# Performance work log

Hardware: AMD Instinct MI355X
Metric: run time of the kernel (lower is better)

## Reference

```python
import jax, jax.numpy as jnp
import numpy as np

IN_C = 256
INTER_C = 64  # in_c // k, k=4
B, H, W = 8, 32, 32
N_TERMS = 5   # numSeriesTerms; numTraceSamples = 1


def setup_inputs():
    key = jax.random.key(0)
    ks = jax.random.split(key, 10)
    s = 0.05
    return {
        "x": jax.random.normal(ks[0], (B, IN_C, H, W), jnp.float32),
        "Wq": jax.random.normal(ks[1], (INTER_C, IN_C), jnp.float32) * s,
        "bq": jax.random.normal(ks[2], (INTER_C,), jnp.float32) * s,
        "Wk": jax.random.normal(ks[3], (INTER_C, IN_C), jnp.float32) * s,
        "bk": jax.random.normal(ks[4], (INTER_C,), jnp.float32) * s,
        "Wc": jax.random.normal(ks[5], (2 * INTER_C,), jnp.float32) * s,
        "Wv": jax.random.normal(ks[6], (IN_C, IN_C), jnp.float32) * s,
        "bv": jax.random.normal(ks[7], (IN_C,), jnp.float32) * s,
        "gamma": jnp.full((1,), 0.5, jnp.float32),
        "u": jax.random.normal(ks[8], (B, IN_C, H, W), jnp.float32),
    }


def _attention(x, Wq, bq, Wk, bk, Wc, Wv, bv, gamma):
    # Attention_concat.forward. concat_conv is a bias-free linear map over the
    # channel concat, so energy[i,j] = <Wc[:ic], q_i> + <Wc[ic:], k_j> exactly.
    b, c, h, w = x.shape
    n = h * w
    xf = x.reshape(b, c, n)                                   # [B,C,N]
    q = jnp.einsum('oc,bcn->bon', Wq, xf) + bq[None, :, None]  # [B,ic,N]
    k = jnp.einsum('oc,bcn->bon', Wk, xf) + bk[None, :, None]  # [B,ic,N]
    ic = Wq.shape[0]
    eq = jnp.einsum('c,bcn->bn', Wc[:ic], q)                  # [B,N]
    ek = jnp.einsum('c,bcn->bn', Wc[ic:], k)                  # [B,N]
    attn = (eq[:, :, None] + ek[:, None, :]) / n              # energy/(H*W), [B,N,N]
    v = jnp.einsum('oc,bcn->bon', Wv, xf) + bv[None, :, None]  # [B,C,N]
    out = jnp.einsum('bcn,bnm->bcm', v, attn).reshape(b, c, h, w)
    return gamma * out + x


def _forward(x, Wq, bq, Wk, bk, Wc, Wv, bv, gamma, u):
    att = lambda z, g: _attention(z, Wq, bq, Wk, bk, Wc, Wv, bv, g)
    # turbulance_hook: runs under torch.no_grad and rescales gamma in-place
    res = att(x, gamma)
    turbu = att(x * 1.0000001, gamma)
    lip = jnp.linalg.norm(turbu - res) / jnp.linalg.norm(x * 1.0000001 - x)
    factor = jax.lax.stop_gradient(jnp.where(lip > 0.9, 0.9 / lip, 1.0))
    gamma_eff = gamma * factor
    Fx, vjp_fn = jax.vjp(lambda z: att(z, gamma_eff), x)
    # power_series_matrix_logarithm_trace: Hutchinson estimate of
    # tr(log(I+J)) ~= sum_j (-1)^{j+1}/j * u^T J^j u, 1 probe, 5 terms
    b = x.shape[0]
    uf = u.reshape(b, -1)
    vcur = u
    tr = jnp.zeros((b,), x.dtype)
    for j in range(1, N_TERMS + 1):
        vcur = vjp_fn(vcur)[0]                 # u^T J^j via repeated vjp
        dot = jnp.sum(vcur.reshape(b, -1) * uf, axis=1)
        tr = tr + ((-1.0) ** (j + 1) / j) * dot
    return x + Fx, tr


def reference(x, Wq, bq, Wk, bk, Wc, Wv, bv, gamma, u):
    return _forward(x, Wq, bq, Wk, bk, Wc, Wv, bv, gamma, u)
```

## Files before the change

### kernel.cpp

```cpp
#include <hip/hip_runtime.h>
#include <math.h>

#define NB 8
#define NC 256
#define NN 1024
#define NICH 64

#define WS_AQ    0
#define WS_AK    256
#define WS_MOM2  520
#define WS_SX    1024
#define WS_XE    3072
#define WS_XK    5120
#define WS_T1P   7424
#define WS_T2P   7488
#define WS_VSU   7680
#define WS_UE    9728
#define WS_VEU   11776
#define WS_CAQ   13824
#define WS_CAK   15872
#define WS_CUAK  17920
#define WS_STAT  20480
#define STAT_STRIDE 2560
#define ST_EK    1024
#define ST_SV    2048
#define ST_SVE   2304
#define WS_EQP2  57344
#define WS_EKP2  73728
#define WS_MAQP2 90112
#define WS_MAKP2 106496
#define WS_SX2P  123904
#define WS_UUP   124160
#define WS_WVB   124416

__device__ __forceinline__ float dot4(const float4& a, const float4& b) {
    return a.x * b.x + a.y * b.y + a.z * b.z + a.w * b.w;
}
__device__ __forceinline__ float sum4(const float4& a) {
    return a.x + a.y + a.z + a.w;
}
__device__ __forceinline__ unsigned int bf16lo(float v) {
    unsigned int u = __float_as_uint(v);
    return (u + 0x7FFFu + ((u >> 16) & 1u)) >> 16;
}
__device__ __forceinline__ unsigned int bf16hi(float v) {
    unsigned int u = __float_as_uint(v);
    return (u + 0x7FFFu + ((u >> 16) & 1u)) & 0xFFFF0000u;
}
__device__ __forceinline__ float tolo(unsigned int u) {
    return __uint_as_float(u << 16);
}
__device__ __forceinline__ float tohi(unsigned int u) {
    return __uint_as_float(u & 0xFFFF0000u);
}

__global__ void kA(const float* __restrict__ x, const float* __restrict__ u,
                   const float* __restrict__ Wq, const float* __restrict__ Wk,
                   const float* __restrict__ Wc, const float* __restrict__ Wv,
                   float* __restrict__ ws) {
    const int bid = blockIdx.x;
    const int t = threadIdx.x;
    if (bid >= 256) {
        const int j = bid - 256;
        unsigned int* wvb = (unsigned int*)ws + WS_WVB;
#pragma unroll
        for (int r = 0; r < 4; ++r) {
            int e = j * 1024 + r * 256 + t;
            int q = e >> 13, i = (e >> 8) & 31, o = e & 255;
            float w0 = Wv[(size_t)(q * 64 + 2 * i) * NC + o];
            float w1 = Wv[(size_t)(q * 64 + 2 * i + 1) * NC + o];
            wvb[e] = bf16lo(w0) | bf16hi(w1);
        }
        return;
    }
    const int b = bid >> 5, r = bid & 31;
    const int nq = r >> 1, ch = r & 1;
    __shared__ float aql[128], akl[128];
    __shared__ float red[4][4][64];
    {
        const int c_local = t >> 1, half = t & 1;
        const int cg = ch * 128 + c_local;
        float a = 0.f, k = 0.f;
#pragma unroll 8
        for (int i = 0; i < 32; ++i) {
            int o = half * 32 + i;
            a += Wc[o] * Wq[o * NC + cg];
            k += Wc[64 + o] * Wk[o * NC + cg];
        }
        a += __shfl_xor(a, 1, 64);
        k += __shfl_xor(k, 1, 64);
        if (half == 0) {
            aql[c_local] = a; akl[c_local] = k;
            if (nq == 0) { ws[WS_AQ + cg] = a; ws[WS_AK + cg] = k; }
        }
    }
    __syncthreads();
    const int col = t & 63, grp = t >> 6;
    const int n = nq * 64 + col;
    const float* xb = x + ((size_t)b * NC + ch * 128 + grp * 32) * NN + n;
    const float* ub = u + ((size_t)b * NC + ch * 128 + grp * 32) * NN + n;
    float eqp = 0.f, ekp = 0.f, map = 0.f, mkp = 0.f;
#pragma unroll 8
    for (int i = 0; i < 32; ++i) {
        float xv = xb[(size_t)i * NN];
        float uv = ub[(size_t)i * NN];
        float a = aql[grp * 32 + i], kk = akl[grp * 32 + i];
        eqp += a * xv; ekp += kk * xv;
        map += a * uv; mkp += kk * uv;
    }
    red[grp][0][col] = eqp; red[grp][1][col] = ekp;
    red[grp][2][col] = map; red[grp][3][col] = mkp;
    __syncthreads();
    if (t < 64) {
        int idx = (b * 2 + ch) * 1024 + nq * 64 + t;
        ws[WS_EQP2  + idx] = red[0][0][t] + red[1][0][t] + red[2][0][t] + red[3][0][t];
        ws[WS_EKP2  + idx] = red[0][1][t] + red[1][1][t] + red[2][1][t] + red[3][1][t];
        ws[WS_MAQP2 + idx] = red[0][2][t] + red[1][2][t] + red[2][2][t] + red[3][2][t];
        ws[WS_MAKP2 + idx] = red[0][3][t] + red[1][3][t] + red[2][3][t] + red[3][3][t];
    }
}

__global__ void kB(const float* __restrict__ x, const float* __restrict__ u,
                   const float* __restrict__ Wc, const float* __restrict__ bq,
                   const float* __restrict__ bk, float* __restrict__ ws) {
    const int bid = blockIdx.x;
    const int b = bid >> 5, g = bid & 31;
    const int c0 = g * 8;
    const int t = threadIdx.x;
    const int wid = t >> 6, lane = t & 63;
    __shared__ float s_cq, s_ck;
    __shared__ float mred[4][4];
    __shared__ float wv9[8][9][4];
    __shared__ float accw[2][4];
    if (t < 64) {
        float p = Wc[t] * bq[t], rr = Wc[64 + t] * bk[t];
        for (int off = 32; off > 0; off >>= 1) {
            p += __shfl_down(p, off, 64);
            rr += __shfl_down(rr, off, 64);
        }
        if (t == 0) { s_cq = p; s_ck = rr; }
    }
    __syncthreads();
    const float cq = s_cq, ck = s_ck;
    float4 e4, k4, ma4, mk4;
    {
        float4 a0 = ((const float4*)(ws + WS_EQP2 + (size_t)(b * 2) * 1024))[t];
        float4 a1 = ((const float4*)(ws + WS_EQP2 + (size_t)(b * 2 + 1) * 1024))[t];
        e4.x = a0.x + a1.x + cq; e4.y = a0.y + a1.y + cq;
        e4.z = a0.z + a1.z + cq; e4.w = a0.w + a1.w + cq;
        a0 = ((const float4*)(ws + WS_EKP2 + (size_t)(b * 2) * 1024))[t];
        a1 = ((const float4*)(ws + WS_EKP2 + (size_t)(b * 2 + 1) * 1024))[t];
        k4.x = a0.x + a1.x + ck; k4.y = a0.y + a1.y + ck;
        k4.z = a0.z + a1.z + ck; k4.w = a0.w + a1.w + ck;
        a0 = ((const float4*)(ws + WS_MAQP2 + (size_t)(b * 2) * 1024))[t];
        a1 = ((const float4*)(ws + WS_MAQP2 + (size_t)(b * 2 + 1) * 1024))[t];
        ma4.x = a0.x + a1.x; ma4.y = a0.y + a1.y; ma4.z = a0.z + a1.z; ma4.w = a0.w + a1.w;
        a0 = ((const float4*)(ws + WS_MAKP2 + (size_t)(b * 2) * 1024))[t];
        a1 = ((const float4*)(ws + WS_MAKP2 + (size_t)(b * 2 + 1) * 1024))[t];
        mk4.x = a0.x + a1.x; mk4.y = a0.y + a1.y; mk4.z = a0.z + a1.z; mk4.w = a0.w + a1.w;
    }
    {
        float d0 = sum4(e4), d1 = sum4(k4), d2 = dot4(k4, k4), d3 = dot4(e4, k4);
        for (int off = 32; off > 0; off >>= 1) {
            d0 += __shfl_down(d0, off, 64);
            d1 += __shfl_down(d1, off, 64);
            d2 += __shfl_down(d2, off, 64);
            d3 += __shfl_down(d3, off, 64);
        }
        if (lane == 0) { mred[0][wid] = d0; mred[1][wid] = d1; mred[2][wid] = d2; mred[3][wid] = d3; }
    }
    __syncthreads();
    if (t == 0)
        for (int m = 0; m < 4; ++m)
            ws[WS_MOM2 + b * 4 + m] = mred[m][0] + mred[m][1] + mred[m][2] + mred[m][3];
    if (g == 0)
        ((float4*)(ws + WS_STAT + b * STAT_STRIDE + ST_EK))[t] = k4;
    const float4* xb4 = (const float4*)(x + ((size_t)b * NC + c0) * NN);
    const float4* ub4 = (const float4*)(u + ((size_t)b * NC + c0) * NN);
    float x2a = 0.f, uua = 0.f;
#pragma unroll
    for (int c = 0; c < 8; ++c) {
        float4 xv = xb4[c * 256 + t];
        float4 uv = ub4[c * 256 + t];
        float d[9];
        d[0] = dot4(xv, e4);
        d[1] = dot4(xv, k4);
        d[2] = sum4(uv);
        d[3] = dot4(uv, e4);
        d[4] = dot4(uv, k4);
        d[5] = dot4(xv, ma4);
        d[6] = dot4(xv, mk4);
        d[7] = dot4(uv, mk4);
        d[8] = sum4(xv);
        x2a += dot4(xv, xv);
        uua += dot4(uv, uv);
        for (int off = 32; off > 0; off >>= 1)
            for (int m = 0; m < 9; ++m) d[m] += __shfl_down(d[m], off, 64);
        if (lane == 0) for (int m = 0; m < 9; ++m) wv9[c][m][wid] = d[m];
    }
    for (int off = 32; off > 0; off >>= 1) {
        x2a += __shfl_down(x2a, off, 64);
        uua += __shfl_down(uua, off, 64);
    }
    if (lane == 0) { accw[0][wid] = x2a; accw[1][wid] = uua; }
    __syncthreads();
    if (t < 8) {
        int c = t;
        float v[9];
        for (int m = 0; m < 9; ++m)
            v[m] = wv9[c][m][0] + wv9[c][m][1] + wv9[c][m][2] + wv9[c][m][3];
        ws[WS_XE   + b * NC + c0 + c] = v[0];
        ws[WS_XK   + b * NC + c0 + c] = v[1];
        ws[WS_VSU  + b * NC + c0 + c] = v[2];
        ws[WS_UE   + b * NC + c0 + c] = v[3];
        ws[WS_VEU  + b * NC + c0 + c] = v[4];
        ws[WS_CAQ  + b * NC + c0 + c] = v[5];
        ws[WS_CAK  + b * NC + c0 + c] = v[6];
        ws[WS_CUAK + b * NC + c0 + c] = v[7];
        ws[WS_SX   + b * NC + c0 + c] = v[8];
    }
    if (t == 0) {
        ws[WS_SX2P + bid] = accw[0][0] + accw[0][1] + accw[0][2] + accw[0][3];
        ws[WS_UUP + bid]  = accw[1][0] + accw[1][1] + accw[1][2] + accw[1][3];
    }
}

__global__ void ksv(const float* __restrict__ Wv, const float* __restrict__ bv,
                    const float* __restrict__ Wc, const float* __restrict__ bq,
                    const float* __restrict__ bk, float* __restrict__ ws) {
    const int bid = blockIdx.x;
    const int b = bid >> 3, oc = bid & 7;
    const int t = threadIdx.x;
    const int o_sub = t >> 3, ks = t & 7;
    const int o = oc * 32 + o_sub;
    __shared__ float sxl[NC], xel[NC];
    __shared__ float T1s[32], T2s[32];
    __shared__ float s_cq, s_ck;
    if (t < 64) {
        float p = Wc[t] * bq[t], rr = Wc[64 + t] * bk[t];
        for (int off = 32; off > 0; off >>= 1) {
            p += __shfl_down(p, off, 64);
            rr += __shfl_down(rr, off, 64);
        }
        if (t == 0) { s_cq = p; s_ck = rr; }
    }
    sxl[t] = ws[WS_SX + b * NC + t];
    xel[t] = ws[WS_XE + b * NC + t];
    __syncthreads();
    const float Seq  = ws[WS_MOM2 + b * 4 + 0];
    const float Sek  = ws[WS_MOM2 + b * 4 + 1];
    const float Sek2 = ws[WS_MOM2 + b * 4 + 2];
    const float cq = s_cq, ck = s_ck;
    float wsx = 0.f, wxe = 0.f;
    const float4* wrow = (const float4*)(Wv + (size_t)o * NC);
#pragma unroll
    for (int i = 0; i < 8; ++i) {
        float4 w4 = wrow[i * 8 + ks];
        int k = i * 32 + ks * 4;
        wsx += w4.x * sxl[k] + w4.y * sxl[k + 1] + w4.z * sxl[k + 2] + w4.w * sxl[k + 3];
        wxe += w4.x * xel[k] + w4.y * xel[k + 1] + w4.z * xel[k + 2] + w4.w * xel[k + 3];
    }
    for (int off = 4; off > 0; off >>= 1) {
        wsx += __shfl_down(wsx, off, 8);
        wxe += __shfl_down(wxe, off, 8);
    }
    if (ks == 0) {
        float bvc = bv[o];
        float Sv  = wsx + (float)NN * bvc;
        float SvL = wsx;
        float Sve = wxe + bvc * Seq;
        float* st = ws + WS_STAT + b * STAT_STRIDE;
        st[ST_SV + o] = Sv; st[ST_SVE + o] = Sve;
        float A = 2.f * Sve - bvc * Seq - cq * Sv;
        float sx = sxl[o];
        float xk = ws[WS_XK + b * NC + o];
        float xkL = xk - ck * sx;
        float T1c = A * sx + Sv * xkL + SvL * xk;
        float SP  = Sek - (float)NN * ck;
        float SP2 = Sek2 - 2.f * ck * Sek + (float)NN * ck * ck;
        float SPQ = Sek2 - ck * Sek;
        float T2c = (float)NN * A * A + Sv * Sv * SP2 + SvL * SvL * Sek2
                  + 2.f * A * Sv * SP + 2.f * A * SvL * Sek + 2.f * Sv * SvL * SPQ;
        T1s[o_sub] = T1c; T2s[o_sub] = T2c;
    }
    __syncthreads();
    if (t == 0) {
        float t1 = 0.f, t2 = 0.f;
        for (int i = 0; i < 32; ++i) { t1 += T1s[i]; t2 += T2s[i]; }
        ws[WS_T1P + bid] = t1;
        ws[WS_T2P + bid] = t2;
    }
}

struct KFSMem {
    unsigned int Wlds[32768];
    unsigned int VVb[NC] __attribute__((aligned(16)));
    float redPR[2048];
    float dred[9][4];
    float gred0[4];
    float gredT[2];
    float sge;
};

__global__ void __launch_bounds__(1024, 4) kfin(
        const float* __restrict__ x, const float* __restrict__ bv,
        const float* __restrict__ gamma, float* __restrict__ ws,
        float* __restrict__ out) {
    __shared__ __align__(16) unsigned char smem_raw[sizeof(KFSMem)];
    KFSMem& S = *(KFSMem*)smem_raw;
    const int bid = blockIdx.x;
    const int t = threadIdx.x;
    const int lane = t & 63;
    const bool is_iter = (bid < 8);
    uint4 stg0, stg1, stg2, stg3, stg4, stg5, stg6, stg7;
    if (is_iter) {
        const uint4* wvb4 = (const uint4*)((const unsigned int*)ws + WS_WVB);
        stg0 = wvb4[0 * 1024 + t]; stg1 = wvb4[1 * 1024 + t];
        stg2 = wvb4[2 * 1024 + t]; stg3 = wvb4[3 * 1024 + t];
        stg4 = wvb4[4 * 1024 + t]; stg5 = wvb4[5 * 1024 + t];
        stg6 = wvb4[6 * 1024 + t]; stg7 = wvb4[7 * 1024 + t];
    }
    {
        float a = 0.f, b1 = 0.f, c1 = 0.f;
        if (t < 256) a = ws[WS_SX2P + t];
        if (t < 64) { b1 = ws[WS_T1P + t]; c1 = ws[WS_T2P + t]; }
        for (int off = 32; off > 0; off >>= 1) {
            a  += __shfl_down(a,  off, 64);
            b1 += __shfl_down(b1, off, 64);
            c1 += __shfl_down(c1, off, 64);
        }
        if (t < 256 && lane == 0) S.gred0[t >> 6] = a;
        if (t == 0) { S.gredT[0] = b1; S.gredT[1] = c1; }
    }
    __syncthreads();
    if (t == 0) {
        float S1 = S.gred0[0] + S.gred0[1] + S.gred0[2] + S.gred0[3];
        float inv = gamma[0] * (1.f / (float)NN);
        float dd = S1 + 2.f * inv * S.gredT[0] + inv * inv * S.gredT[1];
        float lip = sqrtf(dd / S1);
        S.sge = gamma[0] * ((lip > 0.9f) ? (0.9f / lip) : 1.f);
    }
    __syncthreads();
    const float ge = S.sge;

    if (!is_iter) {
        const float gn = ge * (1.f / (float)NN);
        const int r = t >> 8, tc = t & 255;
        const int bid2 = (bid - 8) * 4 + r;
        const int b = bid2 >> 8, c = bid2 & 255;
        const float* st = ws + WS_STAT + b * STAT_STRIDE;
        float sv = st[ST_SV + c], sve = st[ST_SVE + c];
        float4 ek4 = ((const float4*)(st + ST_EK))[tc];
        size_t i4 = (size_t)bid2 * 256 + tc;
        float4 x4 = ((const float4*)x)[i4];
        float4 o;
        o.x = 2.f * x4.x + gn * (sve + ek4.x * sv);
        o.y = 2.f * x4.y + gn * (sve + ek4.y * sv);
        o.z = 2.f * x4.z + gn * (sve + ek4.z * sv);
        o.w = 2.f * x4.w + gn * (sve + ek4.w * sv);
        ((float4*)out)[i4] = o;
        return;
    }

    const int b = bid;
    const int o = t & 255, q = t >> 8;
    const int wid4 = o >> 6;
    ((uint4*)S.Wlds)[0 * 1024 + t] = stg0; ((uint4*)S.Wlds)[1 * 1024 + t] = stg1;
    ((uint4*)S.Wlds)[2 * 1024 + t] = stg2; ((uint4*)S.Wlds)[3 * 1024 + t] = stg3;
    ((uint4*)S.Wlds)[4 * 1024 + t] = stg4; ((uint4*)S.Wlds)[5 * 1024 + t] = stg5;
    ((uint4*)S.Wlds)[6 * 1024 + t] = stg6; ((uint4*)S.Wlds)[7 * 1024 + t] = stg7;
    const float s = ge * (1.f / (float)NN);
    float Svl_r = 0.f, sxl_r = 0.f, xkl_r = 0.f, caql_r = 0.f, cakl_r = 0.f,
          Uel_r = 0.f, Vsul_r = 0.f, bvl_r = 0.f, aql_r = 0.f, akl_r = 0.f,
          veu_r = 0.f, cuak_r = 0.f, vsreg = 0.f, vereg = 0.f;
    if (t < 256) {
        const float* st = ws + WS_STAT + b * STAT_STRIDE;
        Svl_r  = st[ST_SV + t];
        sxl_r  = ws[WS_SX   + b * NC + t];
        xkl_r  = ws[WS_XK   + b * NC + t];
        caql_r = ws[WS_CAQ  + b * NC + t];
        cakl_r = ws[WS_CAK  + b * NC + t];
        Uel_r  = ws[WS_UE   + b * NC + t];
        Vsul_r = ws[WS_VSU  + b * NC + t];
        veu_r  = ws[WS_VEU  + b * NC + t];
        cuak_r = ws[WS_CUAK + b * NC + t];
        aql_r  = ws[WS_AQ + t];
        akl_r  = ws[WS_AK + t];
        bvl_r  = bv[t];
        vsreg = Vsul_r; vereg = veu_r;
        S.VVb[t] = bf16lo(vsreg) | bf16hi(vereg);
    }
    const float Seq  = ws[WS_MOM2 + b * 4 + 0];
    const float Sek  = ws[WS_MOM2 + b * 4 + 1];
    const float Sekq = ws[WS_MOM2 + b * 4 + 3];
    float uu = 0.f;
    for (int g = 0; g < 32; ++g) uu += ws[WS_UUP + b * 32 + g];
    __syncthreads();
    if (t < 256) {
        float d[8] = {Svl_r * cuak_r, aql_r * Vsul_r, akl_r * Vsul_r, akl_r * Uel_r,
                      Svl_r * Vsul_r, Svl_r * veu_r,  Svl_r * aql_r,  Svl_r * akl_r};
        for (int off = 32; off > 0; off >>= 1)
            for (int m = 0; m < 8; ++m) d[m] += __shfl_down(d[m], off, 64);
        if (lane == 0) for (int m = 0; m < 8; ++m) S.dred[m][wid4] = d[m];
    }
    __syncthreads();
    float g2a = 0.f, aqVsu = 0.f, akVsu = 0.f, akUe = 0.f, SvVsu = 0.f, SvVeu = 0.f,
          Svaq = 0.f, Svak = 0.f;
    if (t < 256) {
        g2a   = S.dred[0][0] + S.dred[0][1] + S.dred[0][2] + S.dred[0][3];
        aqVsu = S.dred[1][0] + S.dred[1][1] + S.dred[1][2] + S.dred[1][3];
        akVsu = S.dred[2][0] + S.dred[2][1] + S.dred[2][2] + S.dred[2][3];
        akUe  = S.dred[3][0] + S.dred[3][1] + S.dred[3][2] + S.dred[3][3];
        SvVsu = S.dred[4][0] + S.dred[4][1] + S.dred[4][2] + S.dred[4][3];
        SvVeu = S.dred[5][0] + S.dred[5][1] + S.dred[5][2] + S.dred[5][3];
        Svaq  = S.dred[6][0] + S.dred[6][1] + S.dred[6][2] + S.dred[6][3];
        Svak  = S.dred[7][0] + S.dred[7][1] + S.dred[7][2] + S.dred[7][3];
    }
    __syncthreads();
    const float lam = 1.f + s * Svak;
    float alpha = 1.f, beta = 0.f, gam = 0.f;
    float SxAcc = 0.f, XkAcc = 0.f, CakAcc = 0.f;
    float dot = uu, tr = 0.f;
    const float coef[5] = {1.f, -0.5f, 1.f / 3.f, -0.25f, 0.2f};
    for (int j = 0; j < 5; ++j) {
        float pa = 0.f, ra = 0.f;
#pragma unroll
        for (int kk = 0; kk < 8; ++kk) {
            const int base = (q * 32 + 4 * kk) * 256 + o;
            unsigned int w0 = S.Wlds[base];
            unsigned int w1 = S.Wlds[base + 256];
            unsigned int w2 = S.Wlds[base + 512];
            unsigned int w3 = S.Wlds[base + 768];
            uint4 va = ((const uint4*)S.VVb)[q * 16 + 2 * kk];
            uint4 vb = ((const uint4*)S.VVb)[q * 16 + 2 * kk + 1];
            pa += tolo(w0) * tolo(va.x) + tohi(w0) * tolo(va.y);
            ra += tolo(w0) * tohi(va.x) + tohi(w0) * tohi(va.y);
            pa += tolo(w1) * tolo(va.z) + tohi(w1) * tolo(va.w);
            ra += tolo(w1) * tohi(va.z) + tohi(w1) * tohi(va.w);
            pa += tolo(w2) * tolo(vb.x) + tohi(w2) * tolo(vb.y);
            ra += tolo(w2) * tohi(vb.x) + tohi(w2) * tohi(vb.y);
            pa += tolo(w3) * tolo(vb.z) + tohi(w3) * tolo(vb.w);
            ra += tolo(w3) * tohi(vb.z) + tohi(w3) * tohi(vb.w);
        }
        S.redPR[2 * t] = pa; S.redPR[2 * t + 1] = ra;
        __syncthreads();
        if (t < 256) {
            float Pv = s * (S.redPR[2 * t] + S.redPR[2 * (t + 256)] + S.redPR[2 * (t + 512)] + S.redPR[2 * (t + 768)]);
            float Rv = s * (S.redPR[2 * t + 1] + S.redPR[2 * (t + 256) + 1] + S.redPR[2 * (t + 512) + 1] + S.redPR[2 * (t + 768) + 1]);
            float d[9];
            d[0] = Svl_r * Pv;
            d[1] = Svl_r * Rv;
            d[2] = bvl_r * vsreg;
            d[3] = sxl_r * Pv;
            d[4] = xkl_r * Pv;
            d[5] = caql_r * Pv;
            d[6] = cakl_r * Pv;
            d[7] = Uel_r * Pv;
            d[8] = Vsul_r * Rv;
            for (int off = 32; off > 0; off >>= 1)
                for (int m = 0; m < 9; ++m) d[m] += __shfl_down(d[m], off, 64);
            if (lane == 0) for (int m = 0; m < 9; ++m) S.dred[m][wid4] = d[m];
            __syncthreads();
            float sm[9];
            for (int m = 0; m < 9; ++m)
                sm[m] = S.dred[m][0] + S.dred[m][1] + S.dred[m][2] + S.dred[m][3];
            const float svP = sm[0], svR = sm[1], bvVs = sm[2], sxP = sm[3], xkP = sm[4],
                        caqP = sm[5], cakP = sm[6], ueP = sm[7], vsuR = sm[8];
            const float sB = s * bvVs;
            float St  = s * (alpha * SvVsu + beta * (float)NN + gam * Seq  + Svaq * SxAcc);
            float tek = s * (alpha * SvVeu + beta * Sek        + gam * Sekq + Svaq * XkAcc);
            float uta = s * (alpha * g2a   + beta * akVsu      + gam * akUe + Svaq * CakAcc);
            dot += ueP + caqP + sB * aqVsu + uta + vsuR;
            tr  += coef[j] * dot;
            float nVs = vsreg + Pv * Seq  + aql_r * (sxP + (float)NN * sB) + akl_r * St  + Rv * (float)NN;
            float nVe = vereg + Pv * Sekq + aql_r * (xkP + sB * Sek)       + akl_r * tek + Rv * Sek;
            vsreg = nVs; vereg = nVe;
            S.VVb[t] = bf16lo(nVs) | bf16hi(nVe);
            SxAcc  = lam * SxAcc  + sxP;
            XkAcc  = lam * XkAcc  + xkP;
            CakAcc = lam * CakAcc + cakP;
            beta = lam * beta + Svaq * sB + svR;
            gam  = lam * gam + svP;
            alpha *= lam;
        } else {
            __syncthreads();
        }
        __syncthreads();
    }
    if (t == 0) out[2097152 + b] = tr;
}

extern "C" void kernel_launch(void* const* d_in, const int* in_sizes, int n_in,
                              void* d_out, int out_size, void* d_ws, size_t ws_size,
                              hipStream_t stream) {
    const float* x     = (const float*)d_in[0];
    const float* Wq    = (const float*)d_in[1];
    const float* bq    = (const float*)d_in[2];
    const float* Wk    = (const float*)d_in[3];
    const float* bk    = (const float*)d_in[4];
    const float* Wc    = (const float*)d_in[5];
    const float* Wv    = (const float*)d_in[6];
    const float* bv    = (const float*)d_in[7];
    const float* gamma = (const float*)d_in[8];
    const float* u     = (const float*)d_in[9];
    float* out = (float*)d_out;
    float* ws  = (float*)d_ws;

    kA  <<<dim3(288), dim3(256),  0, stream>>>(x, u, Wq, Wk, Wc, Wv, ws);
    kB  <<<dim3(256), dim3(256),  0, stream>>>(x, u, Wc, bq, bk, ws);
    ksv <<<dim3(64),  dim3(256),  0, stream>>>(Wv, bv, Wc, bq, bk, ws);
    kfin<<<dim3(520), dim3(1024), 0, stream>>>(x, bv, gamma, ws, out);
}
```

Before: 55.48 us.

## Use bf16 MFMA for the iterative Wv matvec with a swizzled weight layout

The per-iteration Wv^T·[Vs,Ve] product in kfin moves from scalar bf16-unpack FMAs plus a cross-thread LDS reduction to 16x16x32 bf16 MFMA instructions. Each wave computes 16 output channels, with rows 0 and 1 of the A fragment holding Vs and Ve and the rest zeroed. kA is reworked to transpose Wv through a shared tile and write it in an XOR-swizzled MFMA-friendly layout, using 4 blocks instead of 32. This removes the redPR reduction, but 14 of 16 MFMA rows are wasted and the changed weight layout must match between kA staging and the kfin reads.

Result: faster. 46.16 us (-16.8%).

```diff
diff --git a/kernel.cpp b/kernel.cpp
--- a/kernel.cpp
+++ b/kernel.cpp
@@ -33,6 +33,10 @@
 #define WS_UUP   124160
 #define WS_WVB   124416
 
+typedef short bf16x8 __attribute__((ext_vector_type(8)));
+typedef float f32x4 __attribute__((ext_vector_type(4)));
+union FragU { uint4 u; bf16x8 h; };
+
 __device__ __forceinline__ float dot4(const float4& a, const float4& b) {
     return a.x * b.x + a.y * b.y + a.z * b.z + a.w * b.w;
 }
@@ -46,12 +50,6 @@
 __device__ __forceinline__ unsigned int bf16hi(float v) {
     unsigned int u = __float_as_uint(v);
     return (u + 0x7FFFu + ((u >> 16) & 1u)) & 0xFFFF0000u;
-}
-__device__ __forceinline__ float tolo(unsigned int u) {
-    return __uint_as_float(u << 16);
-}
-__device__ __forceinline__ float tohi(unsigned int u) {
-    return __uint_as_float(u & 0xFFFF0000u);
 }
 
 __global__ void kA(const float* __restrict__ x, const float* __restrict__ u,
@@ -60,23 +58,36 @@
                    float* __restrict__ ws) {
     const int bid = blockIdx.x;
     const int t = threadIdx.x;
+    __shared__ float tile[256][65];
+    __shared__ float aql[128], akl[128];
+    __shared__ float red[4][4][64];
     if (bid >= 256) {
-        const int j = bid - 256;
-        unsigned int* wvb = (unsigned int*)ws + WS_WVB;
+        const int o0 = (bid - 256) * 64;
+        const int cho = t >> 6, ol = t & 63;
+#pragma unroll 8
+        for (int p = 0; p < 64; ++p) {
+            int ch = p * 4 + cho;
+            tile[ch][ol] = Wv[(size_t)ch * NC + o0 + ol];
+        }
+        __syncthreads();
+        uint4* wvb4 = (uint4*)((unsigned int*)ws + WS_WVB);
 #pragma unroll
-        for (int r = 0; r < 4; ++r) {
-            int e = j * 1024 + r * 256 + t;
-            int q = e >> 13, i = (e >> 8) & 31, o = e & 255;
-            float w0 = Wv[(size_t)(q * 64 + 2 * i) * NC + o];
-            float w1 = Wv[(size_t)(q * 64 + 2 * i + 1) * NC + o];
-            wvb[e] = bf16lo(w0) | bf16hi(w1);
+        for (int i = 0; i < 8; ++i) {
+            int idx = i * 256 + t;
+            int o_l = idx >> 5, s = idx & 31;
+            int o = o0 + o_l;
+            int g = s ^ (o & 7);
+            uint4 out;
+            out.x = bf16lo(tile[8 * g + 0][o_l]) | bf16hi(tile[8 * g + 1][o_l]);
+            out.y = bf16lo(tile[8 * g + 2][o_l]) | bf16hi(tile[8 * g + 3][o_l]);
+            out.z = bf16lo(tile[8 * g + 4][o_l]) | bf16hi(tile[8 * g + 5][o_l]);
+            out.w = bf16lo(tile[8 * g + 6][o_l]) | bf16hi(tile[8 * g + 7][o_l]);
+            wvb4[(size_t)(bid - 256) * 2048 + idx] = out;
         }
         return;
     }
     const int b = bid >> 5, r = bid & 31;
     const int nq = r >> 1, ch = r & 1;
-    __shared__ float aql[128], akl[128];
-    __shared__ float red[4][4][64];
     {
         const int c_local = t >> 1, half = t & 1;
         const int cg = ch * 128 + c_local;
@@ -294,8 +305,10 @@
 
 struct KFSMem {
     unsigned int Wlds[32768];
-    unsigned int VVb[NC] __attribute__((aligned(16)));
-    float redPR[2048];
+    unsigned int Vsb[128] __attribute__((aligned(16)));
+    unsigned int Veb[128] __attribute__((aligned(16)));
+    float P_lds[256];
+    float R_lds[256];
     float dred[9][4];
     float gred0[4];
     float gredT[2];
@@ -363,8 +376,11 @@
     }
 
     const int b = bid;
-    const int o = t & 255, q = t >> 8;
-    const int wid4 = o >> 6;
+    const int nt = t >> 6;
+    const int row = lane & 15;
+    const int kgrp = lane >> 4;
+    const int o = nt * 16 + row;
+    const int wid4 = (t & 255) >> 6;
     ((uint4*)S.Wlds)[0 * 1024 + t] = stg0; ((uint4*)S.Wlds)[1 * 1024 + t] = stg1;
     ((uint4*)S.Wlds)[2 * 1024 + t] = stg2; ((uint4*)S.Wlds)[3 * 1024 + t] = stg3;
     ((uint4*)S.Wlds)[4 * 1024 + t] = stg4; ((uint4*)S.Wlds)[5 * 1024 + t] = stg5;
@@ -388,7 +404,12 @@
         akl_r  = ws[WS_AK + t];
         bvl_r  = bv[t];
         vsreg = Vsul_r; vereg = veu_r;
-        S.VVb[t] = bf16lo(vsreg) | bf16hi(vereg);
+        float vs_o = __shfl_xor(vsreg, 1, 64);
+        float ve_o = __shfl_xor(vereg, 1, 64);
+        if ((t & 1) == 0) {
+            S.Vsb[t >> 1] = bf16lo(vsreg) | bf16hi(vs_o);
+            S.Veb[t >> 1] = bf16lo(vereg) | bf16hi(ve_o);
+        }
     }
     const float Seq  = ws[WS_MOM2 + b * 4 + 0];
     const float Sek  = ws[WS_MOM2 + b * 4 + 1];
@@ -422,31 +443,28 @@
     float SxAcc = 0.f, XkAcc = 0.f, CakAcc = 0.f;
     float dot = uu, tr = 0.f;
     const float coef[5] = {1.f, -0.5f, 1.f / 3.f, -0.25f, 0.2f};
+    const uint4* Vsb4 = (const uint4*)S.Vsb;
+    const uint4* Veb4 = (const uint4*)S.Veb;
+    const uint4* Wlds4 = (const uint4*)S.Wlds;
     for (int j = 0; j < 5; ++j) {
-        float pa = 0.f, ra = 0.f;
+        f32x4 acc = {0.f, 0.f, 0.f, 0.f};
 #pragma unroll
-        for (int kk = 0; kk < 8; ++kk) {
-            const int base = (q * 32 + 4 * kk) * 256 + o;
-            unsigned int w0 = S.Wlds[base];
-            unsigned int w1 = S.Wlds[base + 256];
-            unsigned int w2 = S.Wlds[base + 512];
-            unsigned int w3 = S.Wlds[base + 768];
-            uint4 va = ((const uint4*)S.VVb)[q * 16 + 2 * kk];
-            uint4 vb = ((const uint4*)S.VVb)[q * 16 + 2 * kk + 1];
-            pa += tolo(w0) * tolo(va.x) + tohi(w0) * tolo(va.y);
-            ra += tolo(w0) * tohi(va.x) + tohi(w0) * tohi(va.y);
-            pa += tolo(w1) * tolo(va.z) + tohi(w1) * tolo(va.w);
-            ra += tolo(w1) * tohi(va.z) + tohi(w1) * tohi(va.w);
-            pa += tolo(w2) * tolo(vb.x) + tohi(w2) * tolo(vb.y);
-            ra += tolo(w2) * tohi(vb.x) + tohi(w2) * tohi(vb.y);
-            pa += tolo(w3) * tolo(vb.z) + tohi(w3) * tolo(vb.w);
-            ra += tolo(w3) * tohi(vb.z) + tohi(w3) * tohi(vb.w);
-        }
-        S.redPR[2 * t] = pa; S.redPR[2 * t + 1] = ra;
+        for (int kc = 0; kc < 8; ++kc) {
+            const uint4* asrc = (row == 1) ? Veb4 : Vsb4;
+            uint4 araw = asrc[kc * 4 + kgrp];
+            if (row >= 2) { araw.x = 0u; araw.y = 0u; araw.z = 0u; araw.w = 0u; }
+            FragU fa; fa.u = araw;
+            FragU fb; fb.u = Wlds4[o * 32 + ((kc * 4 + kgrp) ^ (o & 7))];
+            acc = __builtin_amdgcn_mfma_f32_16x16x32_bf16(fa.h, fb.h, acc, 0, 0, 0);
+        }
+        if (lane < 16) {
+            S.P_lds[nt * 16 + lane] = acc[0];
+            S.R_lds[nt * 16 + lane] = acc[1];
+        }
         __syncthreads();
         if (t < 256) {
-            float Pv = s * (S.redPR[2 * t] + S.redPR[2 * (t + 256)] + S.redPR[2 * (t + 512)] + S.redPR[2 * (t + 768)]);
-            float Rv = s * (S.redPR[2 * t + 1] + S.redPR[2 * (t + 256) + 1] + S.redPR[2 * (t + 512) + 1] + S.redPR[2 * (t + 768) + 1]);
+            float Pv = s * S.P_lds[t];
+            float Rv = s * S.R_lds[t];
             float d[9];
             d[0] = Svl_r * Pv;
             d[1] = Svl_r * Rv;
@@ -460,7 +478,11 @@
             for (int off = 32; off > 0; off >>= 1)
                 for (int m = 0; m < 9; ++m) d[m] += __shfl_down(d[m], off, 64);
             if (lane == 0) for (int m = 0; m < 9; ++m) S.dred[m][wid4] = d[m];
-            __syncthreads();
+        }
+        __syncthreads();
+        if (t < 256) {
+            float Pv = s * S.P_lds[t];
+            float Rv = s * S.R_lds[t];
             float sm[9];
             for (int m = 0; m < 9; ++m)
                 sm[m] = S.dred[m][0] + S.dred[m][1] + S.dred[m][2] + S.dred[m][3];
@@ -475,15 +497,18 @@
             float nVs = vsreg + Pv * Seq  + aql_r * (sxP + (float)NN * sB) + akl_r * St  + Rv * (float)NN;
             float nVe = vereg + Pv * Sekq + aql_r * (xkP + sB * Sek)       + akl_r * tek + Rv * Sek;
             vsreg = nVs; vereg = nVe;
-            S.VVb[t] = bf16lo(nVs) | bf16hi(nVe);
+            float vs_o = __shfl_xor(nVs, 1, 64);
+            float ve_o = __shfl_xor(nVe, 1, 64);
+            if ((t & 1) == 0) {
+                S.Vsb[t >> 1] = bf16lo(nVs) | bf16hi(vs_o);
+                S.Veb[t >> 1] = bf16lo(nVe) | bf16hi(ve_o);
+            }
             SxAcc  = lam * SxAcc  + sxP;
             XkAcc  = lam * XkAcc  + xkP;
             CakAcc = lam * CakAcc + cakP;
             beta = lam * beta + Svaq * sB + svR;
             gam  = lam * gam + svP;
             alpha *= lam;
-        } else {
-            __syncthreads();
         }
         __syncthreads();
     }
@@ -506,7 +531,7 @@
     float* out = (float*)d_out;
     float* ws  = (float*)d_ws;
 
-    kA  <<<dim3(288), dim3(256),  0, stream>>>(x, u, Wq, Wk, Wc, Wv, ws);
+    kA  <<<dim3(260), dim3(256),  0, stream>>>(x, u, Wq, Wk, Wc, Wv, ws);
     kB  <<<dim3(256), dim3(256),  0, stream>>>(x, u, Wc, bq, bk, ws);
     ksv <<<dim3(64),  dim3(256),  0, stream>>>(Wv, bv, Wc, bq, bk, ws);
     kfin<<<dim3(520), dim3(1024), 0, stream>>>(x, bv, gamma, ws, out);
```
